# Kernel optimization log

Hardware: AMD Instinct MI355X
Metric: run time of the kernel (lower is better)

Reference implementation:

```python
import jax, jax.numpy as jnp
import numpy as np

NA, NB, NG, D = 250000, 500000, 50000, 64
EA, EG = 1000000, 500000


def setup_inputs() -> dict:
    key = jax.random.key(0)
    k = jax.random.split(key, 7)
    return {
        "atom_ft": jax.random.normal(k[0], (NA, D), dtype=jnp.float32),
        "bond_ft": jax.random.normal(k[1], (NB, D), dtype=jnp.float32),
        "global_ft": jax.random.normal(k[2], (NG, D), dtype=jnp.float32),
        "a2b_src": jax.random.randint(k[3], (EA,), 0, NA, dtype=jnp.int32),
        "a2b_dst": jax.random.randint(k[4], (EA,), 0, NB, dtype=jnp.int32),
        "g2b_src": jax.random.randint(k[5], (EG,), 0, NG, dtype=jnp.int32),
        "g2b_dst": jax.random.randint(k[6], (EG,), 0, NB, dtype=jnp.int32),
    }


def _mean_max(src_ft, src, dst, n_dst):
    # copy_u: gather source-node features onto edges, then segment-reduce to dst
    m = src_ft[src]  # [E, D]
    s = jax.ops.segment_sum(m, dst, num_segments=n_dst)  # [n_dst, D]
    cnt = jax.ops.segment_sum(jnp.ones((dst.shape[0], 1), src_ft.dtype), dst,
                              num_segments=n_dst)  # [n_dst, 1]
    mean = s / jnp.maximum(cnt, 1.0)
    mx = jax.ops.segment_max(m, dst, num_segments=n_dst)
    # DGL fills zero-in-degree nodes with 0 for both mean and max
    mx = jnp.where(cnt > 0, mx, 0.0)
    return mean, mx


def reference(atom_ft, bond_ft, global_ft, a2b_src, a2b_dst, g2b_src, g2b_dst):
    nb = bond_ft.shape[0]
    # etype ('atom','a2b','bond')
    mean_a, max_a = _mean_max(atom_ft, a2b_src, a2b_dst, nb)
    ft = jnp.concatenate([bond_ft, mean_a, max_a], axis=1)  # [NB, 3D]
    # etype ('global','g2b','bond') — applied to the widened bond features
    mean_g, max_g = _mean_max(global_ft, g2b_src, g2b_dst, nb)
    ft = jnp.concatenate([ft, mean_g, max_g], axis=1)  # [NB, 5D]
    return (atom_ft, ft, global_ft)
```

## Files before the change

### kernel.cpp

```cpp
#include <hip/hip_runtime.h>

#define NA 250000
#define NB 500000
#define NG 50000
#define DD 64
#define EA_N 1000000
#define EG_N 500000
#define FTC 320
#define NSEG (2 * NB)
#define CAP 8

#define EDGE4_BLKS (((EA_N + EG_N) / 4 + 255) / 256)
#define COPYA_BLKS 1024
#define COPYG_BLKS 128
#define BOND_BLKS (NB / 16)

#define WS_CNT       0
#define WS_SPILL_CNT 1000000
#define WS_OVF_CNT   1000001
#define WS_OVF       1000016
#define WS_SPILL     2000016
#define WS_SLOTS     5000016
#define WS_NEED_B    ((size_t)(5000016 + (size_t)NSEG * CAP) * 4)

#define SPILL_MAX 1500000

typedef float vf4 __attribute__((ext_vector_type(4)));


__device__ __forceinline__ float4 f4add(float4 a, float4 b) {
    return make_float4(a.x + b.x, a.y + b.y, a.z + b.z, a.w + b.w);
}
__device__ __forceinline__ float4 f4max(float4 a, float4 b) {
    return make_float4(fmaxf(a.x, b.x), fmaxf(a.y, b.y),
                       fmaxf(a.z, b.z), fmaxf(a.w, b.w));
}
__device__ __forceinline__ float4 f4scale(float4 a, float s) {
    return make_float4(a.x * s, a.y * s, a.z * s, a.w * s);
}
__device__ __forceinline__ float4 ntload4(const float4* p) {
    vf4 v = __builtin_nontemporal_load((const vf4*)p);
    return make_float4(v.x, v.y, v.z, v.w);
}
__device__ __forceinline__ void ntstore4(float4 a, float4* p) {
    vf4 v = {a.x, a.y, a.z, a.w};
    __builtin_nontemporal_store(v, (vf4*)p);
}


__global__ __launch_bounds__(256) void bucket_fill_kernel(
    const int4* __restrict__ a2b_src4, const int4* __restrict__ a2b_dst4,
    const int4* __restrict__ g2b_src4, const int4* __restrict__ g2b_dst4,
    int* __restrict__ cnt, int* __restrict__ slots,
    int2* __restrict__ spill, int* __restrict__ ovf,
    int* __restrict__ spill_cnt, int* __restrict__ ovf_cnt) {
    int i = blockIdx.x * blockDim.x + threadIdx.x;
    int stride = gridDim.x * blockDim.x;
    const int totalA = EA_N / 4;
    const int total = (EA_N + EG_N) / 4;
    for (; i < total; i += stride) {
        int4 d, s;
        int base;
        if (i < totalA) {
            d = a2b_dst4[i]; s = a2b_src4[i]; base = 0;
        } else {
            d = g2b_dst4[i - totalA]; s = g2b_src4[i - totalA]; base = NB;
        }
#define PUT(DX, SX)                                                         \
        {                                                                   \
            int seg = base + (DX);                                          \
            int pos = atomicAdd(&cnt[seg], 1);                              \
            if (pos < CAP) {                                                \
                slots[(size_t)seg * CAP + pos] = (SX);                      \
            } else {                                                        \
                int r = atomicAdd(spill_cnt, 1);                            \
                if (r < SPILL_MAX) spill[r] = make_int2(seg, (SX));         \
                if (pos == CAP) { int o = atomicAdd(ovf_cnt, 1); ovf[o] = seg; } \
            }                                                               \
        }
        PUT(d.x, s.x) PUT(d.y, s.y) PUT(d.z, s.z) PUT(d.w, s.w)
#undef PUT
    }
}


__global__ __launch_bounds__(256) void bond_copy_kernel(
    const float4* __restrict__ bond4, const float4* __restrict__ atom4,
    const float4* __restrict__ glob4, const int* __restrict__ cnt,
    const int* __restrict__ slots, float4* __restrict__ ft4,
    float4* __restrict__ out_atom4, float4* __restrict__ out_glob4) {
    int bid = blockIdx.x;

    if (bid < BOND_BLKS) {
        long long b = (long long)bid * 16 + (threadIdx.x >> 4);
        int q = threadIdx.x & 15;
        int gbase = threadIdx.x & 48;

        int da = cnt[b];
        int dg = cnt[NB + b];
        int ia = (q < CAP) ? slots[(size_t)b * CAP + q] : 0;
        int ig = (q < CAP) ? slots[(size_t)(NB + b) * CAP + q] : 0;
        float4 bv = ntload4(&bond4[b * 16 + q]);

        int na = min(da, CAP);
        int ng = min(dg, CAP);

        float4 sa = make_float4(0.f, 0.f, 0.f, 0.f), sg = sa;
        float4 xa = make_float4(-INFINITY, -INFINITY, -INFINITY, -INFINITY), xg = xa;

        for (int j = 0; j < na; ++j) {
            int s = __shfl(ia, gbase + j, 64);
            float4 v = atom4[(long long)s * 16 + q];
            sa = f4add(sa, v);
            xa = f4max(xa, v);
        }
        for (int j = 0; j < ng; ++j) {
            int s = __shfl(ig, gbase + j, 64);
            float4 v = glob4[(long long)s * 16 + q];
            sg = f4add(sg, v);
            xg = f4max(xg, v);
        }

        float4 ma = f4scale(sa, da ? 1.f / (float)da : 0.f);
        float4 mg = f4scale(sg, dg ? 1.f / (float)dg : 0.f);
        if (!da) xa = make_float4(0.f, 0.f, 0.f, 0.f);
        if (!dg) xg = make_float4(0.f, 0.f, 0.f, 0.f);

        float4* row = ft4 + b * 80;
        ntstore4(bv, &row[q]);
        if (da <= CAP) {
            ntstore4(ma, &row[16 + q]);
            ntstore4(xa, &row[32 + q]);
        }
        if (dg <= CAP) {
            ntstore4(mg, &row[48 + q]);
            ntstore4(xg, &row[64 + q]);
        }
    } else if (bid < BOND_BLKS + COPYA_BLKS) {
        long long n4 = (long long)NA * DD / 4;
        long long i = (long long)(bid - BOND_BLKS) * 256 + threadIdx.x;
        long long stride = (long long)COPYA_BLKS * 256;
        for (; i < n4; i += stride) {
            float4 v = ntload4(&atom4[i]);
            ntstore4(v, &out_atom4[i]);
        }
    } else {
        long long n4 = (long long)NG * DD / 4;
        long long i = (long long)(bid - BOND_BLKS - COPYA_BLKS) * 256 + threadIdx.x;
        long long stride = (long long)COPYG_BLKS * 256;
        for (; i < n4; i += stride) {
            float4 v = ntload4(&glob4[i]);
            ntstore4(v, &out_glob4[i]);
        }
    }
}


__global__ __launch_bounds__(256) void redo_kernel(
    const int* __restrict__ cnt, const int* __restrict__ slots,
    const int2* __restrict__ spill, const int* __restrict__ spill_cnt,
    const int* __restrict__ ovf, const int* __restrict__ ovf_cnt,
    const float* __restrict__ atom, const float* __restrict__ glob,
    float* __restrict__ ft) {
    int nov = *ovf_cnt;
    if (nov == 0) return;
    int nsp = min(*spill_cnt, SPILL_MAX);
    int wid = (int)((blockIdx.x * blockDim.x + threadIdx.x) >> 6);
    int lane = threadIdx.x & 63;
    int nw = (gridDim.x * blockDim.x) >> 6;

    for (int o = wid; o < nov; o += nw) {
        int seg = ovf[o];
        int et = (seg >= NB) ? 1 : 0;
        const float* sft = et ? glob : atom;
        int deg = cnt[seg];

        float sum = 0.f, mx = -INFINITY;
        for (int j = 0; j < CAP; ++j) {
            int s = slots[(size_t)seg * CAP + j];
            float v = sft[(size_t)s * DD + lane];
            sum += v; mx = fmaxf(mx, v);
        }
        for (int base = 0; base < nsp; base += 64) {
            int e = base + lane;
            int sseg = -1, ssrc = 0;
            if (e < nsp) { int2 p = spill[e]; sseg = p.x; ssrc = p.y; }
            unsigned long long m = __ballot(sseg == seg);
            while (m) {
                int l = __ffsll((unsigned long long)m) - 1;
                m &= m - 1;
                int s = __shfl(ssrc, l, 64);
                float v = sft[(size_t)s * DD + lane];
                sum += v; mx = fmaxf(mx, v);
            }
        }
        float mean = sum / (float)deg;
        long long b = et ? (seg - NB) : seg;
        float* row = ft + b * (long long)FTC + (et ? 192 : 64);
        row[lane] = mean;
        row[64 + lane] = mx;
    }
}


__device__ __forceinline__ unsigned float_to_key(float f) {
    unsigned u = __float_as_uint(f);
    return (u & 0x80000000u) ? ~u : (u | 0x80000000u);
}
__device__ __forceinline__ float key_to_float(unsigned k) {
    unsigned u = (k & 0x80000000u) ? (k & 0x7FFFFFFFu) : ~k;
    return __uint_as_float(u);
}

__global__ void fb_copy_kernel(const float4* __restrict__ src,
                               float4* __restrict__ dst, long long n4) {
    long long i = (long long)blockIdx.x * blockDim.x + threadIdx.x;
    long long stride = (long long)gridDim.x * blockDim.x;
    for (; i < n4; i += stride) dst[i] = src[i];
}

__global__ void fb_init_ft_kernel(const float4* __restrict__ bond,
                                  float4* __restrict__ ft) {
    const long long n4 = (long long)NB * 80;
    long long i = (long long)blockIdx.x * blockDim.x + threadIdx.x;
    long long stride = (long long)gridDim.x * blockDim.x;
    for (; i < n4; i += stride) {
        long long b = i / 80;
        int c4 = (int)(i - b * 80);
        float4 v = make_float4(0.f, 0.f, 0.f, 0.f);
        if (c4 < 16) v = bond[b * 16 + c4];
        ft[i] = v;
    }
}

__global__ void fb_scatter_kernel(const float* __restrict__ src_ft,
                                  const int* __restrict__ src_idx,
                                  const int* __restrict__ dst_idx,
                                  int n_edges, float* __restrict__ ft,
                                  int sum_col, int max_col,
                                  int* __restrict__ cnt) {
    long long total = (long long)n_edges * 64;
    long long i = (long long)blockIdx.x * blockDim.x + threadIdx.x;
    long long stride = (long long)gridDim.x * blockDim.x;
    for (; i < total; i += stride) {
        int e = (int)(i >> 6);
        int d = (int)(i & 63);
        int s = src_idx[e];
        int b = dst_idx[e];
        float v = src_ft[(long long)s * DD + d];
        atomicAdd(&ft[(long long)b * FTC + sum_col + d], v);
        atomicMax((unsigned*)&ft[(long long)b * FTC + max_col + d], float_to_key(v));
        if (d == 0) atomicAdd(&cnt[b], 1);
    }
}

__global__ void fb_finalize_kernel(float* __restrict__ ft,
                                   const int* __restrict__ cnt_a,
                                   const int* __restrict__ cnt_g) {
    long long total = (long long)NB * 64;
    long long i = (long long)blockIdx.x * blockDim.x + threadIdx.x;
    long long stride = (long long)gridDim.x * blockDim.x;
    for (; i < total; i += stride) {
        long long b = i >> 6;
        int d = (int)(i & 63);
        float* row = ft + b * FTC;
        int ca = cnt_a[b];
        row[64 + d] = row[64 + d] / fmaxf((float)ca, 1.0f);
        unsigned ka = __float_as_uint(row[128 + d]);
        row[128 + d] = (ca > 0) ? key_to_float(ka) : 0.0f;
        int cg = cnt_g[b];
        row[192 + d] = row[192 + d] / fmaxf((float)cg, 1.0f);
        unsigned kg = __float_as_uint(row[256 + d]);
        row[256 + d] = (cg > 0) ? key_to_float(kg) : 0.0f;
    }
}


extern "C" void kernel_launch(void* const* d_in, const int* in_sizes, int n_in,
                              void* d_out, int out_size, void* d_ws, size_t ws_size,
                              hipStream_t stream) {
    const float* atom_ft   = (const float*)d_in[0];
    const float* bond_ft   = (const float*)d_in[1];
    const float* global_ft = (const float*)d_in[2];
    const int* a2b_src = (const int*)d_in[3];
    const int* a2b_dst = (const int*)d_in[4];
    const int* g2b_src = (const int*)d_in[5];
    const int* g2b_dst = (const int*)d_in[6];

    float* out = (float*)d_out;
    float* out_atom = out;
    float* out_ft   = out + (long long)NA * DD;
    float* out_glob = out_ft + (long long)NB * FTC;

    int* ws = (int*)d_ws;
    const int BLK = 256;

    if (ws_size >= WS_NEED_B) {
        int* cnt       = ws + WS_CNT;
        int* spill_cnt = ws + WS_SPILL_CNT;
        int* ovf_cnt   = ws + WS_OVF_CNT;
        int* ovf       = ws + WS_OVF;
        int2* spill    = (int2*)(ws + WS_SPILL);
        int* slots     = ws + WS_SLOTS;

        (void)hipMemsetAsync(cnt, 0, (size_t)(WS_OVF) * 4, stream);

        bucket_fill_kernel<<<EDGE4_BLKS, BLK, 0, stream>>>(
            (const int4*)a2b_src, (const int4*)a2b_dst,
            (const int4*)g2b_src, (const int4*)g2b_dst,
            cnt, slots, spill, ovf, spill_cnt, ovf_cnt);

        bond_copy_kernel<<<BOND_BLKS + COPYA_BLKS + COPYG_BLKS, BLK, 0, stream>>>(
            (const float4*)bond_ft, (const float4*)atom_ft,
            (const float4*)global_ft, cnt, slots, (float4*)out_ft,
            (float4*)out_atom, (float4*)out_glob);

        redo_kernel<<<64, BLK, 0, stream>>>(
            cnt, slots, spill, spill_cnt, ovf, ovf_cnt,
            atom_ft, global_ft, out_ft);
    } else {
        int* cnt_a = ws;
        int* cnt_g = ws + NB;
        (void)hipMemsetAsync(ws, 0, 2 * (size_t)NB * sizeof(int), stream);
        fb_copy_kernel<<<4096, BLK, 0, stream>>>(
            (const float4*)atom_ft, (float4*)out_atom, (long long)NA * DD / 4);
        fb_copy_kernel<<<2048, BLK, 0, stream>>>(
            (const float4*)global_ft, (float4*)out_glob, (long long)NG * DD / 4);
        fb_init_ft_kernel<<<8192, BLK, 0, stream>>>(
            (const float4*)bond_ft, (float4*)out_ft);
        fb_scatter_kernel<<<8192, BLK, 0, stream>>>(
            atom_ft, a2b_src, a2b_dst, EA_N, out_ft, 64, 128, cnt_a);
        fb_scatter_kernel<<<8192, BLK, 0, stream>>>(
            global_ft, g2b_src, g2b_dst, EG_N, out_ft, 192, 256, cnt_g);
        fb_finalize_kernel<<<8192, BLK, 0, stream>>>(out_ft, cnt_a, cnt_g);
    }
}
```

Baseline: 333.4 us.

## Move feature copies into bucket-fill kernel and fold overflow redo into bond kernel

The atom and global passthrough copies move out of the bond kernel and into the bucket-fill launch. The bandwidth-bound copies can then overlap with the atomic-latency-bound edge bucketing. The separate overflow redo kernel is merged into the bond kernel as extra trailing blocks, which removes one launch. Each lane now does a single slot-index load that covers both edge types instead of two. This is safe only because bond blocks skip writing overflowed segments, which the redo blocks fill in; the fused kernels carry more branching and resource pressure.

```diff
diff --git a/kernel.cpp b/kernel.cpp
--- a/kernel.cpp
+++ b/kernel.cpp
@@ -14,6 +14,7 @@
 #define COPYA_BLKS 1024
 #define COPYG_BLKS 128
 #define BOND_BLKS (NB / 16)
+#define REDO_BLKS 64
 
 #define WS_CNT       0
 #define WS_SPILL_CNT 1000000
@@ -48,47 +49,71 @@
 }
 
 
-__global__ __launch_bounds__(256) void bucket_fill_kernel(
+__global__ __launch_bounds__(256) void bucket_fill_copy_kernel(
     const int4* __restrict__ a2b_src4, const int4* __restrict__ a2b_dst4,
     const int4* __restrict__ g2b_src4, const int4* __restrict__ g2b_dst4,
     int* __restrict__ cnt, int* __restrict__ slots,
     int2* __restrict__ spill, int* __restrict__ ovf,
-    int* __restrict__ spill_cnt, int* __restrict__ ovf_cnt) {
-    int i = blockIdx.x * blockDim.x + threadIdx.x;
-    int stride = gridDim.x * blockDim.x;
-    const int totalA = EA_N / 4;
-    const int total = (EA_N + EG_N) / 4;
-    for (; i < total; i += stride) {
-        int4 d, s;
-        int base;
-        if (i < totalA) {
-            d = a2b_dst4[i]; s = a2b_src4[i]; base = 0;
-        } else {
-            d = g2b_dst4[i - totalA]; s = g2b_src4[i - totalA]; base = NB;
-        }
+    int* __restrict__ spill_cnt, int* __restrict__ ovf_cnt,
+    const float4* __restrict__ atom4, float4* __restrict__ out_atom4,
+    const float4* __restrict__ glob4, float4* __restrict__ out_glob4) {
+    int bid = blockIdx.x;
+
+    if (bid < EDGE4_BLKS) {
+        int i = bid * blockDim.x + threadIdx.x;
+        const int totalA = EA_N / 4;
+        const int total = (EA_N + EG_N) / 4;
+        if (i < total) {
+            int4 d, s;
+            int base;
+            if (i < totalA) {
+                d = a2b_dst4[i]; s = a2b_src4[i]; base = 0;
+            } else {
+                d = g2b_dst4[i - totalA]; s = g2b_src4[i - totalA]; base = NB;
+            }
 #define PUT(DX, SX)                                                         \
-        {                                                                   \
-            int seg = base + (DX);                                          \
-            int pos = atomicAdd(&cnt[seg], 1);                              \
-            if (pos < CAP) {                                                \
-                slots[(size_t)seg * CAP + pos] = (SX);                      \
-            } else {                                                        \
-                int r = atomicAdd(spill_cnt, 1);                            \
-                if (r < SPILL_MAX) spill[r] = make_int2(seg, (SX));         \
-                if (pos == CAP) { int o = atomicAdd(ovf_cnt, 1); ovf[o] = seg; } \
-            }                                                               \
-        }
-        PUT(d.x, s.x) PUT(d.y, s.y) PUT(d.z, s.z) PUT(d.w, s.w)
+            {                                                               \
+                int seg = base + (DX);                                      \
+                int pos = atomicAdd(&cnt[seg], 1);                          \
+                if (pos < CAP) {                                            \
+                    slots[(size_t)seg * CAP + pos] = (SX);                  \
+                } else {                                                    \
+                    int r = atomicAdd(spill_cnt, 1);                        \
+                    if (r < SPILL_MAX) spill[r] = make_int2(seg, (SX));     \
+                    if (pos == CAP) { int o = atomicAdd(ovf_cnt, 1); ovf[o] = seg; } \
+                }                                                           \
+            }
+            PUT(d.x, s.x) PUT(d.y, s.y) PUT(d.z, s.z) PUT(d.w, s.w)
 #undef PUT
-    }
-}
-
-
-__global__ __launch_bounds__(256) void bond_copy_kernel(
+        }
+    } else if (bid < EDGE4_BLKS + COPYA_BLKS) {
+        long long n4 = (long long)NA * DD / 4;
+        long long i = (long long)(bid - EDGE4_BLKS) * 256 + threadIdx.x;
+        long long stride = (long long)COPYA_BLKS * 256;
+        for (; i < n4; i += stride) {
+            float4 v = ntload4(&atom4[i]);
+            ntstore4(v, &out_atom4[i]);
+        }
+    } else {
+        long long n4 = (long long)NG * DD / 4;
+        long long i = (long long)(bid - EDGE4_BLKS - COPYA_BLKS) * 256 + threadIdx.x;
+        long long stride = (long long)COPYG_BLKS * 256;
+        for (; i < n4; i += stride) {
+            float4 v = ntload4(&glob4[i]);
+            ntstore4(v, &out_glob4[i]);
+        }
+    }
+}
+
+
+__global__ __launch_bounds__(256) void bond_redo_kernel(
     const float4* __restrict__ bond4, const float4* __restrict__ atom4,
     const float4* __restrict__ glob4, const int* __restrict__ cnt,
     const int* __restrict__ slots, float4* __restrict__ ft4,
-    float4* __restrict__ out_atom4, float4* __restrict__ out_glob4) {
+    const int2* __restrict__ spill, const int* __restrict__ spill_cnt,
+    const int* __restrict__ ovf, const int* __restrict__ ovf_cnt,
+    const float* __restrict__ atom, const float* __restrict__ glob,
+    float* __restrict__ ft) {
     int bid = blockIdx.x;
 
     if (bid < BOND_BLKS) {
@@ -98,8 +123,9 @@
 
         int da = cnt[b];
         int dg = cnt[NB + b];
-        int ia = (q < CAP) ? slots[(size_t)b * CAP + q] : 0;
-        int ig = (q < CAP) ? slots[(size_t)(NB + b) * CAP + q] : 0;
+        size_t sidx = (q < CAP) ? ((size_t)b * CAP + q)
+                                : ((size_t)(NB + b) * CAP + (q - CAP));
+        int is = slots[sidx];
         float4 bv = ntload4(&bond4[b * 16 + q]);
 
         int na = min(da, CAP);
@@ -109,13 +135,13 @@
         float4 xa = make_float4(-INFINITY, -INFINITY, -INFINITY, -INFINITY), xg = xa;
 
         for (int j = 0; j < na; ++j) {
-            int s = __shfl(ia, gbase + j, 64);
+            int s = __shfl(is, gbase + j, 64);
             float4 v = atom4[(long long)s * 16 + q];
             sa = f4add(sa, v);
             xa = f4max(xa, v);
         }
         for (int j = 0; j < ng; ++j) {
-            int s = __shfl(ig, gbase + j, 64);
+            int s = __shfl(is, gbase + CAP + j, 64);
             float4 v = glob4[(long long)s * 16 + q];
             sg = f4add(sg, v);
             xg = f4max(xg, v);
@@ -136,69 +162,45 @@
             ntstore4(mg, &row[48 + q]);
             ntstore4(xg, &row[64 + q]);
         }
-    } else if (bid < BOND_BLKS + COPYA_BLKS) {
-        long long n4 = (long long)NA * DD / 4;
-        long long i = (long long)(bid - BOND_BLKS) * 256 + threadIdx.x;
-        long long stride = (long long)COPYA_BLKS * 256;
-        for (; i < n4; i += stride) {
-            float4 v = ntload4(&atom4[i]);
-            ntstore4(v, &out_atom4[i]);
-        }
     } else {
-        long long n4 = (long long)NG * DD / 4;
-        long long i = (long long)(bid - BOND_BLKS - COPYA_BLKS) * 256 + threadIdx.x;
-        long long stride = (long long)COPYG_BLKS * 256;
-        for (; i < n4; i += stride) {
-            float4 v = ntload4(&glob4[i]);
-            ntstore4(v, &out_glob4[i]);
-        }
-    }
-}
-
-
-__global__ __launch_bounds__(256) void redo_kernel(
-    const int* __restrict__ cnt, const int* __restrict__ slots,
-    const int2* __restrict__ spill, const int* __restrict__ spill_cnt,
-    const int* __restrict__ ovf, const int* __restrict__ ovf_cnt,
-    const float* __restrict__ atom, const float* __restrict__ glob,
-    float* __restrict__ ft) {
-    int nov = *ovf_cnt;
-    if (nov == 0) return;
-    int nsp = min(*spill_cnt, SPILL_MAX);
-    int wid = (int)((blockIdx.x * blockDim.x + threadIdx.x) >> 6);
-    int lane = threadIdx.x & 63;
-    int nw = (gridDim.x * blockDim.x) >> 6;
-
-    for (int o = wid; o < nov; o += nw) {
-        int seg = ovf[o];
-        int et = (seg >= NB) ? 1 : 0;
-        const float* sft = et ? glob : atom;
-        int deg = cnt[seg];
-
-        float sum = 0.f, mx = -INFINITY;
-        for (int j = 0; j < CAP; ++j) {
-            int s = slots[(size_t)seg * CAP + j];
-            float v = sft[(size_t)s * DD + lane];
-            sum += v; mx = fmaxf(mx, v);
-        }
-        for (int base = 0; base < nsp; base += 64) {
-            int e = base + lane;
-            int sseg = -1, ssrc = 0;
-            if (e < nsp) { int2 p = spill[e]; sseg = p.x; ssrc = p.y; }
-            unsigned long long m = __ballot(sseg == seg);
-            while (m) {
-                int l = __ffsll((unsigned long long)m) - 1;
-                m &= m - 1;
-                int s = __shfl(ssrc, l, 64);
+        int nov = *ovf_cnt;
+        if (nov == 0) return;
+        int nsp = min(*spill_cnt, SPILL_MAX);
+        int wid = (int)(((long long)(bid - BOND_BLKS) * 256 + threadIdx.x) >> 6);
+        int lane = threadIdx.x & 63;
+        int nw = (REDO_BLKS * 256) >> 6;
+
+        for (int o = wid; o < nov; o += nw) {
+            int seg = ovf[o];
+            int et = (seg >= NB) ? 1 : 0;
+            const float* sft = et ? glob : atom;
+            int deg = cnt[seg];
+
+            float sum = 0.f, mx = -INFINITY;
+            for (int j = 0; j < CAP; ++j) {
+                int s = slots[(size_t)seg * CAP + j];
                 float v = sft[(size_t)s * DD + lane];
                 sum += v; mx = fmaxf(mx, v);
             }
-        }
-        float mean = sum / (float)deg;
-        long long b = et ? (seg - NB) : seg;
-        float* row = ft + b * (long long)FTC + (et ? 192 : 64);
-        row[lane] = mean;
-        row[64 + lane] = mx;
+            for (int base = 0; base < nsp; base += 64) {
+                int e = base + lane;
+                int sseg = -1, ssrc = 0;
+                if (e < nsp) { int2 p = spill[e]; sseg = p.x; ssrc = p.y; }
+                unsigned long long m = __ballot(sseg == seg);
+                while (m) {
+                    int l = __ffsll((unsigned long long)m) - 1;
+                    m &= m - 1;
+                    int s = __shfl(ssrc, l, 64);
+                    float v = sft[(size_t)s * DD + lane];
+                    sum += v; mx = fmaxf(mx, v);
+                }
+            }
+            float mean = sum / (float)deg;
+            long long bb = et ? (seg - NB) : seg;
+            float* row = ft + bb * (long long)FTC + (et ? 192 : 64);
+            row[lane] = mean;
+            row[64 + lane] = mx;
+        }
     }
 }
 
@@ -305,19 +307,17 @@
 
         (void)hipMemsetAsync(cnt, 0, (size_t)(WS_OVF) * 4, stream);
 
-        bucket_fill_kernel<<<EDGE4_BLKS, BLK, 0, stream>>>(
+        bucket_fill_copy_kernel<<<EDGE4_BLKS + COPYA_BLKS + COPYG_BLKS, BLK, 0, stream>>>(
             (const int4*)a2b_src, (const int4*)a2b_dst,
             (const int4*)g2b_src, (const int4*)g2b_dst,
-            cnt, slots, spill, ovf, spill_cnt, ovf_cnt);
-
-        bond_copy_kernel<<<BOND_BLKS + COPYA_BLKS + COPYG_BLKS, BLK, 0, stream>>>(
+            cnt, slots, spill, ovf, spill_cnt, ovf_cnt,
+            (const float4*)atom_ft, (float4*)out_atom,
+            (const float4*)global_ft, (float4*)out_glob);
+
+        bond_redo_kernel<<<BOND_BLKS + REDO_BLKS, BLK, 0, stream>>>(
             (const float4*)bond_ft, (const float4*)atom_ft,
             (const float4*)global_ft, cnt, slots, (float4*)out_ft,
-            (float4*)out_atom, (float4*)out_glob);
-
-        redo_kernel<<<64, BLK, 0, stream>>>(
-            cnt, slots, spill, spill_cnt, ovf, ovf_cnt,
-            atom_ft, global_ft, out_ft);
+            spill, spill_cnt, ovf, ovf_cnt, atom_ft, global_ft, out_ft);
     } else {
         int* cnt_a = ws;
         int* cnt_g = ws + NB;
```

Measured after the change: 343.9 us. +3.2%, slower.
